# Kernel tuning notes

Measured on AMD Instinct MI355X. Metric: run time of the kernel, lower is better.

## Reference

```python
import jax, jax.numpy as jnp
import numpy as np

B, S, D_MODEL = 2, 1024, 512
HEAD = 8
DEPTH = D_MODEL // HEAD  # 64
NFEAT = 64


def _make_orf(rng, n_features, depth):
    # Mirrors OrthogonalRandomFeature: QR of uniform blocks, scaled by norms of gaussian rows.
    n, rem = divmod(n_features, depth)
    blocks = []
    for _ in range(n):
        q, _ = np.linalg.qr(rng.random((depth, depth)))
        blocks.append(q)
    if rem > 0:
        q, _ = np.linalg.qr(rng.random((depth, depth)))
        blocks.append(q[:rem])
    orf = np.concatenate(blocks, axis=0)
    mult = np.linalg.norm(rng.standard_normal((n_features, depth)), axis=1)
    return jnp.asarray(mult[:, None] * orf, dtype=jnp.float32)


def setup_inputs() -> dict:
    key = jax.random.key(0)
    ks = jax.random.split(key, 12)
    rng = np.random.default_rng(0)
    scale = 0.02
    inp = {
        "query": jax.random.normal(ks[0], (B, S, D_MODEL), dtype=jnp.float32),
        "key": jax.random.normal(ks[1], (B, S, D_MODEL), dtype=jnp.float32),
        "value": jax.random.normal(ks[2], (B, S, D_MODEL), dtype=jnp.float32),
        "Wq": jax.random.normal(ks[3], (DEPTH, DEPTH), dtype=jnp.float32) * scale,
        "bq": jnp.zeros((DEPTH,), dtype=jnp.float32),
        "Wk": jax.random.normal(ks[4], (DEPTH, DEPTH), dtype=jnp.float32) * scale,
        "bk": jnp.zeros((DEPTH,), dtype=jnp.float32),
        "Wv": jax.random.normal(ks[5], (DEPTH, DEPTH), dtype=jnp.float32) * scale,
        "bv": jnp.zeros((DEPTH,), dtype=jnp.float32),
        "orf_q": _make_orf(rng, NFEAT, DEPTH),
        "orf_k": _make_orf(rng, NFEAT, DEPTH),
        "Wfc": jax.random.normal(ks[6], (D_MODEL, D_MODEL), dtype=jnp.float32) * scale,
        "bfc": jnp.zeros((D_MODEL,), dtype=jnp.float32),
        "causal": 1,
    }
    return inp


def _kernel_fn(x, orf):
    # x: [n,h,s,d], orf: [f,d]; normalization uses ORF.shape[-1] = depth
    norm = 1.0 / (orf.shape[-1] ** 0.25)
    out = jnp.einsum('nhsd,fd->nhsf', x * norm, orf)
    return jax.nn.relu(out) + 0.001


def _causal_attention(q, k, v):
    # q,k: [n,h,s,f]; v: [n,h,s,d]
    k_cumsum = jnp.cumsum(k, axis=-2)                    # [n,h,s,f]
    x = jnp.einsum('nhkf,nhkd->nhkfd', k, v)             # [n,h,s,f,d]
    x = jnp.cumsum(x, axis=-3)
    x = x / k_cumsum[..., None]
    return jnp.einsum('nhqfd,nhqf->nhqd', x, q)          # [n,h,s,d]


def _bidirectional_attention(q, k, v):
    kt_i = jnp.sum(k, axis=-2)                           # [n,h,f]
    norm = 1.0 / jnp.einsum('nhqf,nhf->nhq', q, kt_i)    # [n,h,s]
    k_v = jnp.einsum('nhkf,nhkd->nhfd', k, v)            # [n,h,f,d]
    return jnp.einsum('nhfd,nhqf,nhq->nhqd', k_v, q, norm)


def reference(query, key, value, Wq, bq, Wk, bk, Wv, bv, orf_q, orf_k, Wfc, bfc, causal):
    b, s, _ = query.shape
    depth = Wq.shape[0]
    head = query.shape[-1] // depth
    # [b,s,d_model] -> [b,h,s,depth]
    q = query.reshape(b, s, head, depth).transpose(0, 2, 1, 3)
    k = key.reshape(b, s, head, depth).transpose(0, 2, 1, 3)
    v = value.reshape(b, s, head, depth).transpose(0, 2, 1, 3)
    # per-head Linear on depth (torch: x @ W.T + b)
    q = jnp.einsum('nhsd,ed->nhse', q, Wq) + bq
    k = jnp.einsum('nhsd,ed->nhse', k, Wk) + bk
    v = jnp.einsum('nhsd,ed->nhse', v, Wv) + bv
    q = _kernel_fn(q, orf_q)
    k = _kernel_fn(k, orf_k)
    if causal:
        out = _causal_attention(q, k, v)
    else:
        out = _bidirectional_attention(q, k, v)
    out = out.transpose(0, 2, 1, 3).reshape(b, s, head * depth)
    return jnp.einsum('nse,oe->nso', out, Wfc) + bfc
```

## Files before the change

### kernel.cpp

```cpp
#include <hip/hip_runtime.h>


#define BB 2
#define SS 1024
#define HH 8
#define DD 64
#define FF 64
#define DM 512
#define NCH 16

typedef __bf16 bf16_t;
typedef __attribute__((ext_vector_type(8))) __bf16 bf16x8;
typedef __attribute__((ext_vector_type(4))) __bf16 bf16x4;
typedef __attribute__((ext_vector_type(4))) float f32x4;

#define MFMA16(a,b,c) __builtin_amdgcn_mfma_f32_16x16x32_bf16((a),(b),(c),0,0,0)

__device__ inline bf16x8 cvt_f32x8(const float* p){
    const float4* p4 = (const float4*)p;
    float4 x = p4[0], y = p4[1];
    bf16x8 r;
    r[0]=(__bf16)x.x; r[1]=(__bf16)x.y; r[2]=(__bf16)x.z; r[3]=(__bf16)x.w;
    r[4]=(__bf16)y.x; r[5]=(__bf16)y.y; r[6]=(__bf16)y.z; r[7]=(__bf16)y.w;
    return r;
}

__global__ __launch_bounds__(256) void kfuse(
    const float* __restrict__ orf_q, const float* __restrict__ orf_k,
    const float* __restrict__ Wq, const float* __restrict__ bq,
    const float* __restrict__ Wk, const float* __restrict__ bk,
    const float* __restrict__ Wv, const float* __restrict__ Wfc,
    bf16_t* __restrict__ Mtq, bf16_t* __restrict__ Mtk,
    float* __restrict__ cq, float* __restrict__ ck,
    bf16_t* __restrict__ WvB, bf16_t* __restrict__ WfcB)
{
    const int tid = threadIdx.x, bid = blockIdx.x;
    if (bid < 2) {
        const float* ORF = bid ? orf_k : orf_q;
        const float* W   = bid ? Wk : Wq;
        const float* bb  = bid ? bk : bq;
        bf16_t* Mt = bid ? Mtk : Mtq;
        float* cc  = bid ? ck : cq;
        const float norm = 0.35355339059327373f;
        const int f = tid >> 2, d0 = (tid & 3) * 16;
        float acc[16];
        #pragma unroll
        for (int j=0;j<16;j++) acc[j]=0.f;
        float bacc = 0.f;
        for (int e=0;e<64;e++){
            float oe = ORF[f*64+e];
            const float* wr = W + e*64 + d0;
            #pragma unroll
            for (int j=0;j<16;j++) acc[j] += oe*wr[j];
            bacc += oe*bb[e];
        }
        #pragma unroll
        for (int j=0;j<16;j++) Mt[f*64+d0+j] = (__bf16)(norm*acc[j]);
        if ((tid&3)==0) cc[f] = norm*bacc;
    } else if (bid == 2) {
        for (int i=tid;i<4096;i+=256) WvB[i] = (__bf16)Wv[i];
    } else {
        const float4* W4 = (const float4*)Wfc;
        for (int i=(bid-3)*256+tid; i<65536; i+=13*256){
            float4 v = W4[i];
            bf16x4 o; o[0]=(__bf16)v.x; o[1]=(__bf16)v.y; o[2]=(__bf16)v.z; o[3]=(__bf16)v.w;
            *(bf16x4*)(WfcB + 4*i) = o;
        }
    }
}

__global__ __launch_bounds__(512) void kproj(
    const float* __restrict__ q_in, const float* __restrict__ k_in,
    const float* __restrict__ v_in,
    const bf16_t* __restrict__ Mtq, const float* __restrict__ cq,
    const bf16_t* __restrict__ Mtk, const float* __restrict__ ck,
    const bf16_t* __restrict__ WvB, const float* __restrict__ bv,
    bf16_t* __restrict__ PHI_Q, bf16_t* __restrict__ PHI_K,
    bf16_t* __restrict__ PHI_KT, bf16_t* __restrict__ VPT,
    float* __restrict__ CST, float* __restrict__ KCS)
{
    __shared__ bf16_t kt[64*72];
    __shared__ bf16_t vt[64*72];
    __shared__ float dsT[64*68];
    __shared__ float part[256];
    const int tid = threadIdx.x;
    const int l = tid & 63;
    const int w = __builtin_amdgcn_readfirstlane(tid >> 6);
    const int ww = w & 3;
    const int qd = l >> 4, m = l & 15;
    const int bid = blockIdx.x;
    const int bh = bid >> 4, ch = bid & 15;
    const int b = bh >> 3, h = bh & 7;
    const int s0 = ch*64;
    const int sw = s0 + ww*16;

    if (w < 4) {
        const float* xp = q_in + ((size_t)(b*SS + sw + m))*DM + h*DD;
        bf16x8 a0 = cvt_f32x8(xp + qd*8);
        bf16x8 a1 = cvt_f32x8(xp + 32 + qd*8);
        #pragma unroll
        for (int nt=0;nt<4;nt++){
            const int f = nt*16 + m;
            float cb = cq[f];
            f32x4 acc = {cb,cb,cb,cb};
            acc = MFMA16(a0, *(const bf16x8*)(Mtq + f*64 + qd*8), acc);
            acc = MFMA16(a1, *(const bf16x8*)(Mtq + f*64 + 32 + qd*8), acc);
            #pragma unroll
            for (int r=0;r<4;r++){
                float v = acc[r];
                v = (v>0.f)?v:0.f; v += 0.001f;
                PHI_Q[((size_t)bh*SS + sw + qd*4 + r)*FF + f] = (__bf16)v;
            }
        }
    } else {
        const float* xp = k_in + ((size_t)(b*SS + sw + m))*DM + h*DD;
        bf16x8 a0 = cvt_f32x8(xp + qd*8);
        bf16x8 a1 = cvt_f32x8(xp + 32 + qd*8);
        #pragma unroll
        for (int nt=0;nt<4;nt++){
            const int f = nt*16 + m;
            float cb = ck[f];
            f32x4 acc = {cb,cb,cb,cb};
            acc = MFMA16(a0, *(const bf16x8*)(Mtk + f*64 + qd*8), acc);
            acc = MFMA16(a1, *(const bf16x8*)(Mtk + f*64 + 32 + qd*8), acc);
            #pragma unroll
            for (int r=0;r<4;r++){
                float v = acc[r];
                v = (v>0.f)?v:0.f; v += 0.001f;
                __bf16 h16 = (__bf16)v;
                PHI_K[((size_t)bh*SS + sw + qd*4 + r)*FF + f] = h16;
                kt[f*72 + ww*16 + qd*4 + r] = h16;
            }
        }
    }
    __syncthreads();

    if (tid < 256) {
        const int f = tid >> 2, sg = tid & 3;
        bf16x8 v0 = *(bf16x8*)&kt[f*72 + sg*16];
        bf16x8 v1 = *(bf16x8*)&kt[f*72 + sg*16 + 8];
        bf16_t* dst = PHI_KT + ((size_t)bh*64 + f)*SS + s0 + sg*16;
        *(bf16x8*)dst = v0; *(bf16x8*)(dst+8) = v1;
    } else {
        const float* xp = v_in + ((size_t)(b*SS + sw + m))*DM + h*DD;
        bf16x8 a0 = cvt_f32x8(xp + qd*8);
        bf16x8 a1 = cvt_f32x8(xp + 32 + qd*8);
        #pragma unroll
        for (int nt=0;nt<4;nt++){
            const int e = nt*16 + m;
            float cb = bv[e];
            f32x4 acc = {cb,cb,cb,cb};
            acc = MFMA16(a0, *(const bf16x8*)(WvB + e*64 + qd*8), acc);
            acc = MFMA16(a1, *(const bf16x8*)(WvB + e*64 + 32 + qd*8), acc);
            #pragma unroll
            for (int r=0;r<4;r++)
                vt[e*72 + ww*16 + qd*4 + r] = (__bf16)acc[r];
        }
    }
    __syncthreads();

    {
        const int ft = ww, np = (w >> 2) * 2;
        bf16x8 a0 = *(bf16x8*)&kt[(ft*16+m)*72 + qd*8];
        bf16x8 a1 = *(bf16x8*)&kt[(ft*16+m)*72 + 32 + qd*8];
        #pragma unroll
        for (int j=0;j<2;j++){
            const int nt = np + j;
            f32x4 acc = {0.f,0.f,0.f,0.f};
            acc = MFMA16(a0, *(bf16x8*)&vt[(nt*16+m)*72 + qd*8], acc);
            acc = MFMA16(a1, *(bf16x8*)&vt[(nt*16+m)*72 + 32 + qd*8], acc);
            #pragma unroll
            for (int r=0;r<4;r++)
                dsT[(nt*16+m)*68 + ft*16 + qd*4 + r] = acc[r];
        }
    }
    if (tid < 256) {
        const int d = tid >> 2, sg = tid & 3;
        bf16x8 v0 = *(bf16x8*)&vt[d*72 + sg*16];
        bf16x8 v1 = *(bf16x8*)&vt[d*72 + sg*16 + 8];
        bf16_t* dst = VPT + ((size_t)bh*64 + d)*SS + s0 + sg*16;
        *(bf16x8*)dst = v0; *(bf16x8*)(dst+8) = v1;
    } else {
        const int t2 = tid - 256;
        const int f = t2 & 63, sg = t2 >> 6;
        bf16x8 x0 = *(bf16x8*)&kt[f*72 + sg*16];
        bf16x8 x1 = *(bf16x8*)&kt[f*72 + sg*16 + 8];
        float sm = 0.f;
        #pragma unroll
        for (int j=0;j<8;j++) sm += (float)x0[j] + (float)x1[j];
        part[sg*64 + f] = sm;
    }
    __syncthreads();

    if (tid < 256) {
        const int d = tid >> 2, F = (tid & 3) * 16;
        float* dst = CST + ((size_t)bid*64 + d)*64 + F;
        #pragma unroll
        for (int j=0;j<4;j++)
            *(float4*)(dst + 4*j) = *(float4*)&dsT[d*68 + F + 4*j];
    } else if (tid < 320) {
        const int f = tid - 256;
        KCS[(size_t)bid*64 + f] = part[f] + part[64+f] + part[128+f] + part[192+f];
    }
}

__global__ __launch_bounds__(256) void kprefix(float* __restrict__ CST, float* __restrict__ KCS)
{
    const int tid = threadIdx.x, bid = blockIdx.x;
    const int bh = bid >> 2, q = bid & 3;
    const int e4 = q*256 + tid;
    float4 vals[16];
    #pragma unroll
    for (int c = 0; c < NCH; c++)
        vals[c] = ((float4*)(CST + ((size_t)(bh*NCH + c))*4096))[e4];
    float4 run = make_float4(0.f, 0.f, 0.f, 0.f);
    #pragma unroll
    for (int c = 0; c < NCH; c++) {
        ((float4*)(CST + ((size_t)(bh*NCH + c))*4096))[e4] = run;
        run.x += vals[c].x; run.y += vals[c].y; run.z += vals[c].z; run.w += vals[c].w;
    }
    if (q == 0 && tid < 64) {
        float kv[16];
        #pragma unroll
        for (int c = 0; c < NCH; c++) kv[c] = KCS[((size_t)(bh*NCH + c))*64 + tid];
        float r = 0.f;
        #pragma unroll
        for (int c = 0; c < NCH; c++) { KCS[((size_t)(bh*NCH + c))*64 + tid] = r; r += kv[c]; }
    }
}

__global__ __launch_bounds__(512) void kattn(
    const bf16_t* __restrict__ PHI_Q, const bf16_t* __restrict__ PHI_K,
    const bf16_t* __restrict__ PHI_KT, const bf16_t* __restrict__ VPT,
    const float* __restrict__ CST, const float* __restrict__ KCS,
    bf16_t* __restrict__ O)
{
    __shared__ float kct[64*67];
    __shared__ bf16_t qnl[64*72];
    __shared__ bf16_t sAl[64*72];
    __shared__ float scanp[256];
    const int tid = threadIdx.x;
    const int l = tid & 63;
    const int w = __builtin_amdgcn_readfirstlane(tid >> 6);
    const int rt = w & 3;
    const int np = (w >> 2) * 2;
    const int qd = l >> 4, m = l & 15;
    const int bid = blockIdx.x;
    const int bh = bid >> 4, ch = bid & 15;
    const int cs0 = ch*64;

    if (tid < 256) {
        const int f = tid >> 2, sg = tid & 3;
        const bf16_t* kp = PHI_KT + ((size_t)bh*64 + f)*SS + cs0 + sg*16;
        bf16x8 x0 = *(const bf16x8*)kp;
        bf16x8 x1 = *(const bf16x8*)(kp+8);
        #pragma unroll
        for (int j=0;j<8;j++){
            kct[f*67 + sg*16 + j]     = (float)x0[j];
            kct[f*67 + sg*16 + 8 + j] = (float)x1[j];
        }
    }
    __syncthreads();

    const int f2 = tid >> 2, sg2 = tid & 3;
    float v16[16];
    if (tid < 256) {
        #pragma unroll
        for (int j=0;j<16;j++) v16[j] = kct[f2*67 + sg2*16 + j];
        #pragma unroll
        for (int j=1;j<16;j++) v16[j] += v16[j-1];
        scanp[f2*4 + sg2] = v16[15];
    }
    __syncthreads();
    if (tid < 256) {
        float offs = KCS[(size_t)bid*64 + f2];
        if (sg2 > 0) offs += scanp[f2*4 + 0];
        if (sg2 > 1) offs += scanp[f2*4 + 1];
        if (sg2 > 2) offs += scanp[f2*4 + 2];
        #pragma unroll
        for (int j=0;j<16;j++) kct[f2*67 + sg2*16 + j] = offs + v16[j];
    }
    __syncthreads();

    if (tid < 256) {
        const int sr = tid >> 2, F = (tid & 3) * 16;
        const bf16_t* qp = PHI_Q + ((size_t)bh*SS + cs0 + sr)*FF + F;
        bf16x8 x0 = *(const bf16x8*)qp;
        bf16x8 x1 = *(const bf16x8*)(qp+8);
        bf16x8 o0, o1;
        #pragma unroll
        for (int j=0;j<8;j++){
            o0[j] = (__bf16)((float)x0[j] / kct[(F+j)*67 + sr]);
            o1[j] = (__bf16)((float)x1[j] / kct[(F+8+j)*67 + sr]);
        }
        *(bf16x8*)&qnl[sr*72 + F]     = o0;
        *(bf16x8*)&qnl[sr*72 + F + 8] = o1;
    }
    __syncthreads();

    bf16x8 qa0 = *(bf16x8*)&qnl[(rt*16+m)*72 + qd*8];
    bf16x8 qa1 = *(bf16x8*)&qnl[(rt*16+m)*72 + 32 + qd*8];

    #pragma unroll
    for (int j=0;j<2;j++){
        const int nt = np + j;
        const bf16_t* kb = PHI_K + ((size_t)bh*SS + cs0 + nt*16 + m)*FF;
        f32x4 acc = {0.f,0.f,0.f,0.f};
        acc = MFMA16(qa0, *(const bf16x8*)(kb + qd*8), acc);
        acc = MFMA16(qa1, *(const bf16x8*)(kb + 32 + qd*8), acc);
        const int t_loc = nt*16 + m;
        #pragma unroll
        for (int r=0;r<4;r++){
            const int s_loc = rt*16 + qd*4 + r;
            float v = (t_loc <= s_loc) ? acc[r] : 0.f;
            sAl[s_loc*72 + t_loc] = (__bf16)v;
        }
    }
    __syncthreads();

    bf16x8 sa0 = *(bf16x8*)&sAl[(rt*16+m)*72 + qd*8];
    bf16x8 sa1 = *(bf16x8*)&sAl[(rt*16+m)*72 + 32 + qd*8];

    #pragma unroll
    for (int j=0;j<2;j++){
        const int nt = np + j;
        const int d = nt*16 + m;
        const bf16_t* vb = VPT + ((size_t)bh*64 + d)*SS + cs0;
        const float* pp = CST + ((size_t)bid*64 + d)*64;
        f32x4 acc = {0.f,0.f,0.f,0.f};
        acc = MFMA16(sa0, *(const bf16x8*)(vb + qd*8), acc);
        acc = MFMA16(sa1, *(const bf16x8*)(vb + 32 + qd*8), acc);
        acc = MFMA16(qa0, cvt_f32x8(pp + qd*8), acc);
        acc = MFMA16(qa1, cvt_f32x8(pp + 32 + qd*8), acc);
        #pragma unroll
        for (int r=0;r<4;r++)
            O[((size_t)bh*SS + cs0 + rt*16 + qd*4 + r)*DD + d] = (__bf16)acc[r];
    }
}

__global__ __launch_bounds__(512) void kfc(
    const bf16_t* __restrict__ O, const bf16_t* __restrict__ WfcB,
    const float* __restrict__ bfc, float* __restrict__ out)
{
    const int tid = threadIdx.x;
    const int l = tid & 63;
    const int w = __builtin_amdgcn_readfirstlane(tid >> 6);
    const int rw = w & 3, cpair = (w >> 2) * 2;
    const int qd = l >> 4, m = l & 15;
    const int bid = blockIdx.x;
    const int rb = bid >> 3, cb = bid & 7;
    const int r0 = rb*64 + rw*16;

    f32x4 acc[2];
    #pragma unroll
    for (int j=0;j<2;j++){
        float bb = bfc[cb*64 + (cpair+j)*16 + m];
        acc[j][0]=bb; acc[j][1]=bb; acc[j][2]=bb; acc[j][3]=bb;
    }
    const int row = r0 + m;
    const int b = row >> 10, s = row & 1023;
    #pragma unroll 4
    for (int c=0;c<16;c++){
        const int h = c >> 1;
        const int doff = (c & 1)*32 + qd*8;
        bf16x8 a = *(const bf16x8*)(O + ((size_t)((b*HH + h)*SS + s))*DD + doff);
        #pragma unroll
        for (int j=0;j<2;j++){
            bf16x8 bfr = *(const bf16x8*)(WfcB + (size_t)(cb*64 + (cpair+j)*16 + m)*DM + c*32 + qd*8);
            acc[j] = MFMA16(a, bfr, acc[j]);
        }
    }
    #pragma unroll
    for (int j=0;j<2;j++){
        #pragma unroll
        for (int r=0;r<4;r++){
            const int rr = r0 + qd*4 + r;
            out[(size_t)rr*DM + cb*64 + (cpair+j)*16 + m] = acc[j][r];
        }
    }
}

extern "C" void kernel_launch(void* const* d_in, const int* in_sizes, int n_in,
                              void* d_out, int out_size, void* d_ws, size_t ws_size,
                              hipStream_t stream) {
    const float* q_in  = (const float*)d_in[0];
    const float* k_in  = (const float*)d_in[1];
    const float* v_in  = (const float*)d_in[2];
    const float* Wq    = (const float*)d_in[3];
    const float* bq    = (const float*)d_in[4];
    const float* Wk    = (const float*)d_in[5];
    const float* bk    = (const float*)d_in[6];
    const float* Wv    = (const float*)d_in[7];
    const float* bv    = (const float*)d_in[8];
    const float* orf_q = (const float*)d_in[9];
    const float* orf_k = (const float*)d_in[10];
    const float* Wfc   = (const float*)d_in[11];
    const float* bfc   = (const float*)d_in[12];

    float* CST   = (float*)d_ws;
    float* KCS   = CST + 1048576;
    float* cq    = KCS + 16384;
    float* ck    = cq + 64;
    bf16_t* PHI_Q  = (bf16_t*)(ck + 64);
    bf16_t* PHI_K  = PHI_Q + 1048576;
    bf16_t* PHI_KT = PHI_K + 1048576;
    bf16_t* VPT    = PHI_KT + 1048576;
    bf16_t* O      = VPT + 1048576;
    bf16_t* Mtq    = O + 1048576;
    bf16_t* Mtk    = Mtq + 4096;
    bf16_t* WvB    = Mtk + 4096;
    bf16_t* WfcB   = WvB + 4096;

    kfuse<<<16, 256, 0, stream>>>(orf_q, orf_k, Wq, bq, Wk, bk, Wv, Wfc,
                                  Mtq, Mtk, cq, ck, WvB, WfcB);
    kproj<<<256, 512, 0, stream>>>(q_in, k_in, v_in, Mtq, cq, Mtk, ck, WvB, bv,
                                   PHI_Q, PHI_K, PHI_KT, VPT, CST, KCS);
    kprefix<<<64, 256, 0, stream>>>(CST, KCS);
    kattn<<<256, 512, 0, stream>>>(PHI_Q, PHI_K, PHI_KT, VPT, CST, KCS, O);
    kfc<<<256, 512, 0, stream>>>(O, WfcB, bfc, (float*)d_out);
}
```

Baseline: 134.0 us.

## Fuse all five kernels into one persistent kernel with grid-wide atomic barriers

```diff
diff --git a/kernel.cpp b/kernel.cpp
--- a/kernel.cpp
+++ b/kernel.cpp
@@ -1,7 +1,6 @@
 #include <hip/hip_runtime.h>
 
 
-#define BB 2
 #define SS 1024
 #define HH 8
 #define DD 64
@@ -16,73 +15,55 @@
 
 #define MFMA16(a,b,c) __builtin_amdgcn_mfma_f32_16x16x32_bf16((a),(b),(c),0,0,0)
 
-__device__ inline bf16x8 cvt_f32x8(const float* p){
-    const float4* p4 = (const float4*)p;
-    float4 x = p4[0], y = p4[1];
+__device__ inline bf16x8 pack8(float4 x, float4 y){
     bf16x8 r;
     r[0]=(__bf16)x.x; r[1]=(__bf16)x.y; r[2]=(__bf16)x.z; r[3]=(__bf16)x.w;
     r[4]=(__bf16)y.x; r[5]=(__bf16)y.y; r[6]=(__bf16)y.z; r[7]=(__bf16)y.w;
     return r;
 }
-
-__global__ __launch_bounds__(256) void kfuse(
-    const float* __restrict__ orf_q, const float* __restrict__ orf_k,
+__device__ inline bf16x8 cvt_f32x8(const float* p){
+    const float4* p4 = (const float4*)p;
+    return pack8(p4[0], p4[1]);
+}
+
+__device__ inline void gsync(unsigned* cnt, int slot){
+    __syncthreads();
+    if (threadIdx.x == 0){
+        __threadfence();
+        __hip_atomic_fetch_add(cnt + slot, 1u, __ATOMIC_ACQ_REL, __HIP_MEMORY_SCOPE_AGENT);
+        while (__hip_atomic_load(cnt + slot, __ATOMIC_ACQUIRE, __HIP_MEMORY_SCOPE_AGENT) < 256u)
+            __builtin_amdgcn_s_sleep(2);
+        __threadfence();
+    }
+    __syncthreads();
+}
+
+__global__ __launch_bounds__(512, 2) void kfused(
+    const float* __restrict__ q_in, const float* __restrict__ k_in,
+    const float* __restrict__ v_in,
     const float* __restrict__ Wq, const float* __restrict__ bq,
     const float* __restrict__ Wk, const float* __restrict__ bk,
-    const float* __restrict__ Wv, const float* __restrict__ Wfc,
+    const float* __restrict__ Wv, const float* __restrict__ bv,
+    const float* __restrict__ orf_q, const float* __restrict__ orf_k,
+    const float* __restrict__ Wfc, const float* __restrict__ bfc,
     bf16_t* __restrict__ Mtq, bf16_t* __restrict__ Mtk,
     float* __restrict__ cq, float* __restrict__ ck,
-    bf16_t* __restrict__ WvB, bf16_t* __restrict__ WfcB)
+    bf16_t* __restrict__ WvB, bf16_t* __restrict__ WfcB,
+    float* __restrict__ CST, float* __restrict__ KCS,
+    bf16_t* __restrict__ O, unsigned* __restrict__ syncc,
+    float* __restrict__ out)
 {
-    const int tid = threadIdx.x, bid = blockIdx.x;
-    if (bid < 2) {
-        const float* ORF = bid ? orf_k : orf_q;
-        const float* W   = bid ? Wk : Wq;
-        const float* bb  = bid ? bk : bq;
-        bf16_t* Mt = bid ? Mtk : Mtq;
-        float* cc  = bid ? ck : cq;
-        const float norm = 0.35355339059327373f;
-        const int f = tid >> 2, d0 = (tid & 3) * 16;
-        float acc[16];
-        #pragma unroll
-        for (int j=0;j<16;j++) acc[j]=0.f;
-        float bacc = 0.f;
-        for (int e=0;e<64;e++){
-            float oe = ORF[f*64+e];
-            const float* wr = W + e*64 + d0;
-            #pragma unroll
-            for (int j=0;j<16;j++) acc[j] += oe*wr[j];
-            bacc += oe*bb[e];
-        }
-        #pragma unroll
-        for (int j=0;j<16;j++) Mt[f*64+d0+j] = (__bf16)(norm*acc[j]);
-        if ((tid&3)==0) cc[f] = norm*bacc;
-    } else if (bid == 2) {
-        for (int i=tid;i<4096;i+=256) WvB[i] = (__bf16)Wv[i];
-    } else {
-        const float4* W4 = (const float4*)Wfc;
-        for (int i=(bid-3)*256+tid; i<65536; i+=13*256){
-            float4 v = W4[i];
-            bf16x4 o; o[0]=(__bf16)v.x; o[1]=(__bf16)v.y; o[2]=(__bf16)v.z; o[3]=(__bf16)v.w;
-            *(bf16x4*)(WfcB + 4*i) = o;
-        }
-    }
-}
-
-__global__ __launch_bounds__(512) void kproj(
-    const float* __restrict__ q_in, const float* __restrict__ k_in,
-    const float* __restrict__ v_in,
-    const bf16_t* __restrict__ Mtq, const float* __restrict__ cq,
-    const bf16_t* __restrict__ Mtk, const float* __restrict__ ck,
-    const bf16_t* __restrict__ WvB, const float* __restrict__ bv,
-    bf16_t* __restrict__ PHI_Q, bf16_t* __restrict__ PHI_K,
-    bf16_t* __restrict__ PHI_KT, bf16_t* __restrict__ VPT,
-    float* __restrict__ CST, float* __restrict__ KCS)
-{
-    __shared__ bf16_t kt[64*72];
-    __shared__ bf16_t vt[64*72];
-    __shared__ float dsT[64*68];
-    __shared__ float part[256];
+    __shared__ __align__(16) char smem[64512];
+    float*  dsT  = (float*)smem;
+    float*  kct  = (float*)smem;
+    bf16_t* kt   = (bf16_t*)(smem + 17408);
+    bf16_t* sAl  = (bf16_t*)(smem + 17408);
+    bf16_t* vt   = (bf16_t*)(smem + 26624);
+    bf16_t* qnl  = (bf16_t*)(smem + 35840);
+    bf16_t* phql = (bf16_t*)(smem + 45056);
+    bf16_t* phkl = (bf16_t*)(smem + 54272);
+    float*  part = (float*)(smem + 63488);
+
     const int tid = threadIdx.x;
     const int l = tid & 63;
     const int w = __builtin_amdgcn_readfirstlane(tid >> 6);
@@ -94,71 +75,110 @@
     const int s0 = ch*64;
     const int sw = s0 + ww*16;
 
-    if (w < 4) {
-        const float* xp = q_in + ((size_t)(b*SS + sw + m))*DM + h*DD;
-        bf16x8 a0 = cvt_f32x8(xp + qd*8);
-        bf16x8 a1 = cvt_f32x8(xp + 32 + qd*8);
-        #pragma unroll
-        for (int nt=0;nt<4;nt++){
-            const int f = nt*16 + m;
-            float cb = cq[f];
-            f32x4 acc = {cb,cb,cb,cb};
-            acc = MFMA16(a0, *(const bf16x8*)(Mtq + f*64 + qd*8), acc);
-            acc = MFMA16(a1, *(const bf16x8*)(Mtq + f*64 + 32 + qd*8), acc);
-            #pragma unroll
-            for (int r=0;r<4;r++){
-                float v = acc[r];
-                v = (v>0.f)?v:0.f; v += 0.001f;
-                PHI_Q[((size_t)bh*SS + sw + qd*4 + r)*FF + f] = (__bf16)v;
-            }
-        }
-    } else {
-        const float* xp = k_in + ((size_t)(b*SS + sw + m))*DM + h*DD;
-        bf16x8 a0 = cvt_f32x8(xp + qd*8);
-        bf16x8 a1 = cvt_f32x8(xp + 32 + qd*8);
-        #pragma unroll
-        for (int nt=0;nt<4;nt++){
-            const int f = nt*16 + m;
-            float cb = ck[f];
-            f32x4 acc = {cb,cb,cb,cb};
-            acc = MFMA16(a0, *(const bf16x8*)(Mtk + f*64 + qd*8), acc);
-            acc = MFMA16(a1, *(const bf16x8*)(Mtk + f*64 + 32 + qd*8), acc);
-            #pragma unroll
-            for (int r=0;r<4;r++){
-                float v = acc[r];
-                v = (v>0.f)?v:0.f; v += 0.001f;
-                __bf16 h16 = (__bf16)v;
-                PHI_K[((size_t)bh*SS + sw + qd*4 + r)*FF + f] = h16;
-                kt[f*72 + ww*16 + qd*4 + r] = h16;
-            }
-        }
-    }
-    __syncthreads();
-
-    if (tid < 256) {
-        const int f = tid >> 2, sg = tid & 3;
-        bf16x8 v0 = *(bf16x8*)&kt[f*72 + sg*16];
-        bf16x8 v1 = *(bf16x8*)&kt[f*72 + sg*16 + 8];
-        bf16_t* dst = PHI_KT + ((size_t)bh*64 + f)*SS + s0 + sg*16;
-        *(bf16x8*)dst = v0; *(bf16x8*)(dst+8) = v1;
-    } else {
-        const float* xp = v_in + ((size_t)(b*SS + sw + m))*DM + h*DD;
-        bf16x8 a0 = cvt_f32x8(xp + qd*8);
-        bf16x8 a1 = cvt_f32x8(xp + 32 + qd*8);
+    const float* xrow = ((w < 4) ? q_in : k_in) + ((size_t)(b*SS + sw + m))*DM + h*DD;
+    float4 pA0 = *(const float4*)(xrow + qd*8);
+    float4 pA1 = *(const float4*)(xrow + qd*8 + 4);
+    float4 pB0 = *(const float4*)(xrow + 32 + qd*8);
+    float4 pB1 = *(const float4*)(xrow + 32 + qd*8 + 4);
+    float4 vA0 = {0,0,0,0}, vA1 = {0,0,0,0}, vB0 = {0,0,0,0}, vB1 = {0,0,0,0};
+    if (w >= 4){
+        const float* vrow = v_in + ((size_t)(b*SS + sw + m))*DM + h*DD;
+        vA0 = *(const float4*)(vrow + qd*8);
+        vA1 = *(const float4*)(vrow + qd*8 + 4);
+        vB0 = *(const float4*)(vrow + 32 + qd*8);
+        vB1 = *(const float4*)(vrow + 32 + qd*8 + 4);
+    }
+
+    if (bid < 2){
+        if (tid < 256){
+            const float* ORF = bid ? orf_k : orf_q;
+            const float* W   = bid ? Wk : Wq;
+            const float* bb  = bid ? bk : bq;
+            bf16_t* Mt = bid ? Mtk : Mtq;
+            float* cc  = bid ? ck : cq;
+            const float norm = 0.35355339059327373f;
+            const int f = tid >> 2, d0 = (tid & 3) * 16;
+            float acc[16];
+            #pragma unroll
+            for (int j=0;j<16;j++) acc[j]=0.f;
+            float bacc = 0.f;
+            for (int e=0;e<64;e++){
+                float oe = ORF[f*64+e];
+                const float* wr = W + e*64 + d0;
+                #pragma unroll
+                for (int j=0;j<16;j++) acc[j] += oe*wr[j];
+                bacc += oe*bb[e];
+            }
+            #pragma unroll
+            for (int j=0;j<16;j++) Mt[f*64+d0+j] = (__bf16)(norm*acc[j]);
+            if ((tid&3)==0) cc[f] = norm*bacc;
+        }
+    } else if (bid == 2){
+        for (int i=tid;i<4096;i+=512) WvB[i] = (__bf16)Wv[i];
+    } else if (bid < 16){
+        const float4* W4 = (const float4*)Wfc;
+        for (int i=(bid-3)*512+tid; i<65536; i+=13*512){
+            float4 v = W4[i];
+            bf16x4 o; o[0]=(__bf16)v.x; o[1]=(__bf16)v.y; o[2]=(__bf16)v.z; o[3]=(__bf16)v.w;
+            *(bf16x4*)(WfcB + 4*i) = o;
+        }
+    }
+    gsync(syncc, 0);
+
+    {
+        bf16x8 a0 = pack8(pA0, pA1);
+        bf16x8 a1 = pack8(pB0, pB1);
+        if (w < 4){
+            #pragma unroll
+            for (int nt=0;nt<4;nt++){
+                const int f = nt*16 + m;
+                float cb = cq[f];
+                f32x4 acc = {cb,cb,cb,cb};
+                acc = MFMA16(a0, *(const bf16x8*)(Mtq + f*64 + qd*8), acc);
+                acc = MFMA16(a1, *(const bf16x8*)(Mtq + f*64 + 32 + qd*8), acc);
+                #pragma unroll
+                for (int r=0;r<4;r++){
+                    float v = acc[r];
+                    v = (v>0.f)?v:0.f; v += 0.001f;
+                    phql[(ww*16 + qd*4 + r)*72 + f] = (__bf16)v;
+                }
+            }
+        } else {
+            #pragma unroll
+            for (int nt=0;nt<4;nt++){
+                const int f = nt*16 + m;
+                float cb = ck[f];
+                f32x4 acc = {cb,cb,cb,cb};
+                acc = MFMA16(a0, *(const bf16x8*)(Mtk + f*64 + qd*8), acc);
+                acc = MFMA16(a1, *(const bf16x8*)(Mtk + f*64 + 32 + qd*8), acc);
+                #pragma unroll
+                for (int r=0;r<4;r++){
+                    float v = acc[r];
+                    v = (v>0.f)?v:0.f; v += 0.001f;
+                    __bf16 h16 = (__bf16)v;
+                    kt[f*72 + ww*16 + qd*4 + r] = h16;
+                    phkl[(ww*16 + qd*4 + r)*72 + f] = h16;
+                }
+            }
+        }
+    }
+    __syncthreads();
+    if (w >= 4){
+        bf16x8 va0 = pack8(vA0, vA1);
+        bf16x8 va1 = pack8(vB0, vB1);
         #pragma unroll
         for (int nt=0;nt<4;nt++){
             const int e = nt*16 + m;
             float cb = bv[e];
             f32x4 acc = {cb,cb,cb,cb};
-            acc = MFMA16(a0, *(const bf16x8*)(WvB + e*64 + qd*8), acc);
-            acc = MFMA16(a1, *(const bf16x8*)(WvB + e*64 + 32 + qd*8), acc);
+            acc = MFMA16(va0, *(const bf16x8*)(WvB + e*64 + qd*8), acc);
+            acc = MFMA16(va1, *(const bf16x8*)(WvB + e*64 + 32 + qd*8), acc);
             #pragma unroll
             for (int r=0;r<4;r++)
                 vt[e*72 + ww*16 + qd*4 + r] = (__bf16)acc[r];
         }
     }
     __syncthreads();
-
     {
         const int ft = ww, np = (w >> 2) * 2;
         bf16x8 a0 = *(bf16x8*)&kt[(ft*16+m)*72 + qd*8];
@@ -174,13 +194,7 @@
                 dsT[(nt*16+m)*68 + ft*16 + qd*4 + r] = acc[r];
         }
     }
-    if (tid < 256) {
-        const int d = tid >> 2, sg = tid & 3;
-        bf16x8 v0 = *(bf16x8*)&vt[d*72 + sg*16];
-        bf16x8 v1 = *(bf16x8*)&vt[d*72 + sg*16 + 8];
-        bf16_t* dst = VPT + ((size_t)bh*64 + d)*SS + s0 + sg*16;
-        *(bf16x8*)dst = v0; *(bf16x8*)(dst+8) = v1;
-    } else {
+    if (tid >= 256){
         const int t2 = tid - 256;
         const int f = t2 & 63, sg = t2 >> 6;
         bf16x8 x0 = *(bf16x8*)&kt[f*72 + sg*16];
@@ -191,69 +205,45 @@
         part[sg*64 + f] = sm;
     }
     __syncthreads();
-
-    if (tid < 256) {
+    if (tid < 256){
         const int d = tid >> 2, F = (tid & 3) * 16;
         float* dst = CST + ((size_t)bid*64 + d)*64 + F;
         #pragma unroll
         for (int j=0;j<4;j++)
             *(float4*)(dst + 4*j) = *(float4*)&dsT[d*68 + F + 4*j];
-    } else if (tid < 320) {
+    } else if (tid < 320){
         const int f = tid - 256;
         KCS[(size_t)bid*64 + f] = part[f] + part[64+f] + part[128+f] + part[192+f];
     }
-}
-
-__global__ __launch_bounds__(256) void kprefix(float* __restrict__ CST, float* __restrict__ KCS)
-{
-    const int tid = threadIdx.x, bid = blockIdx.x;
-    const int bh = bid >> 2, q = bid & 3;
-    const int e4 = q*256 + tid;
-    float4 vals[16];
-    #pragma unroll
-    for (int c = 0; c < NCH; c++)
-        vals[c] = ((float4*)(CST + ((size_t)(bh*NCH + c))*4096))[e4];
-    float4 run = make_float4(0.f, 0.f, 0.f, 0.f);
-    #pragma unroll
-    for (int c = 0; c < NCH; c++) {
-        ((float4*)(CST + ((size_t)(bh*NCH + c))*4096))[e4] = run;
-        run.x += vals[c].x; run.y += vals[c].y; run.z += vals[c].z; run.w += vals[c].w;
-    }
-    if (q == 0 && tid < 64) {
+    gsync(syncc, 1);
+
+    if (tid < 64){
+        const int e4 = ch*64 + tid;
+        float4 vals[16];
+        #pragma unroll
+        for (int c=0;c<NCH;c++)
+            vals[c] = ((float4*)(CST + ((size_t)(bh*NCH + c))*4096))[e4];
+        float4 run = {0.f,0.f,0.f,0.f};
+        #pragma unroll
+        for (int c=0;c<NCH;c++){
+            ((float4*)(CST + ((size_t)(bh*NCH + c))*4096))[e4] = run;
+            run.x += vals[c].x; run.y += vals[c].y; run.z += vals[c].z; run.w += vals[c].w;
+        }
+    } else if (ch == 0 && tid < 128){
+        const int f = tid - 64;
         float kv[16];
         #pragma unroll
-        for (int c = 0; c < NCH; c++) kv[c] = KCS[((size_t)(bh*NCH + c))*64 + tid];
+        for (int c=0;c<NCH;c++) kv[c] = KCS[((size_t)(bh*NCH + c))*64 + f];
         float r = 0.f;
         #pragma unroll
-        for (int c = 0; c < NCH; c++) { KCS[((size_t)(bh*NCH + c))*64 + tid] = r; r += kv[c]; }
-    }
-}
-
-__global__ __launch_bounds__(512) void kattn(
-    const bf16_t* __restrict__ PHI_Q, const bf16_t* __restrict__ PHI_K,
-    const bf16_t* __restrict__ PHI_KT, const bf16_t* __restrict__ VPT,
-    const float* __restrict__ CST, const float* __restrict__ KCS,
-    bf16_t* __restrict__ O)
-{
-    __shared__ float kct[64*67];
-    __shared__ bf16_t qnl[64*72];
-    __shared__ bf16_t sAl[64*72];
-    __shared__ float scanp[256];
-    const int tid = threadIdx.x;
-    const int l = tid & 63;
-    const int w = __builtin_amdgcn_readfirstlane(tid >> 6);
-    const int rt = w & 3;
-    const int np = (w >> 2) * 2;
-    const int qd = l >> 4, m = l & 15;
-    const int bid = blockIdx.x;
-    const int bh = bid >> 4, ch = bid & 15;
-    const int cs0 = ch*64;
-
-    if (tid < 256) {
+        for (int c=0;c<NCH;c++){ KCS[((size_t)(bh*NCH + c))*64 + f] = r; r += kv[c]; }
+    }
+    gsync(syncc, 2);
+
+    if (tid < 256){
         const int f = tid >> 2, sg = tid & 3;
-        const bf16_t* kp = PHI_KT + ((size_t)bh*64 + f)*SS + cs0 + sg*16;
-        bf16x8 x0 = *(const bf16x8*)kp;
-        bf16x8 x1 = *(const bf16x8*)(kp+8);
+        bf16x8 x0 = *(bf16x8*)&kt[f*72 + sg*16];
+        bf16x8 x1 = *(bf16x8*)&kt[f*72 + sg*16 + 8];
         #pragma unroll
         for (int j=0;j<8;j++){
             kct[f*67 + sg*16 + j]     = (float)x0[j];
@@ -261,32 +251,31 @@
         }
     }
     __syncthreads();
-
-    const int f2 = tid >> 2, sg2 = tid & 3;
-    float v16[16];
-    if (tid < 256) {
-        #pragma unroll
-        for (int j=0;j<16;j++) v16[j] = kct[f2*67 + sg2*16 + j];
-        #pragma unroll
-        for (int j=1;j<16;j++) v16[j] += v16[j-1];
-        scanp[f2*4 + sg2] = v16[15];
-    }
-    __syncthreads();
-    if (tid < 256) {
-        float offs = KCS[(size_t)bid*64 + f2];
-        if (sg2 > 0) offs += scanp[f2*4 + 0];
-        if (sg2 > 1) offs += scanp[f2*4 + 1];
-        if (sg2 > 2) offs += scanp[f2*4 + 2];
-        #pragma unroll
-        for (int j=0;j<16;j++) kct[f2*67 + sg2*16 + j] = offs + v16[j];
-    }
-    __syncthreads();
-
-    if (tid < 256) {
+    {
+        const int f2 = tid >> 2, sg2 = tid & 3;
+        float v16[16];
+        if (tid < 256){
+            #pragma unroll
+            for (int j=0;j<16;j++) v16[j] = kct[f2*67 + sg2*16 + j];
+            #pragma unroll
+            for (int j=1;j<16;j++) v16[j] += v16[j-1];
+            part[f2*4 + sg2] = v16[15];
+        }
+        __syncthreads();
+        if (tid < 256){
+            float offs = KCS[(size_t)bid*64 + f2];
+            if (sg2 > 0) offs += part[f2*4 + 0];
+            if (sg2 > 1) offs += part[f2*4 + 1];
+            if (sg2 > 2) offs += part[f2*4 + 2];
+            #pragma unroll
+            for (int j=0;j<16;j++) kct[f2*67 + sg2*16 + j] = offs + v16[j];
+        }
+    }
+    __syncthreads();
+    if (tid < 256){
         const int sr = tid >> 2, F = (tid & 3) * 16;
-        const bf16_t* qp = PHI_Q + ((size_t)bh*SS + cs0 + sr)*FF + F;
-        bf16x8 x0 = *(const bf16x8*)qp;
-        bf16x8 x1 = *(const bf16x8*)(qp+8);
+        bf16x8 x0 = *(bf16x8*)&phql[sr*72 + F];
+        bf16x8 x1 = *(bf16x8*)&phql[sr*72 + F + 8];
         bf16x8 o0, o1;
         #pragma unroll
         for (int j=0;j<8;j++){
@@ -298,16 +287,16 @@
     }
     __syncthreads();
 
+    const int rt = ww, np = (w >> 2) * 2;
     bf16x8 qa0 = *(bf16x8*)&qnl[(rt*16+m)*72 + qd*8];
     bf16x8 qa1 = *(bf16x8*)&qnl[(rt*16+m)*72 + 32 + qd*8];
 
     #pragma unroll
     for (int j=0;j<2;j++){
         const int nt = np + j;
-        const bf16_t* kb = PHI_K + ((size_t)bh*SS + cs0 + nt*16 + m)*FF;
         f32x4 acc = {0.f,0.f,0.f,0.f};
-        acc = MFMA16(qa0, *(const bf16x8*)(kb + qd*8), acc);
-        acc = MFMA16(qa1, *(const bf16x8*)(kb + 32 + qd*8), acc);
+        acc = MFMA16(qa0, *(const bf16x8*)&phkl[(nt*16+m)*72 + qd*8], acc);
+        acc = MFMA16(qa1, *(const bf16x8*)&phkl[(nt*16+m)*72 + 32 + qd*8], acc);
         const int t_loc = nt*16 + m;
         #pragma unroll
         for (int r=0;r<4;r++){
@@ -318,64 +307,56 @@
     }
     __syncthreads();
 
-    bf16x8 sa0 = *(bf16x8*)&sAl[(rt*16+m)*72 + qd*8];
-    bf16x8 sa1 = *(bf16x8*)&sAl[(rt*16+m)*72 + 32 + qd*8];
-
-    #pragma unroll
-    for (int j=0;j<2;j++){
-        const int nt = np + j;
-        const int d = nt*16 + m;
-        const bf16_t* vb = VPT + ((size_t)bh*64 + d)*SS + cs0;
-        const float* pp = CST + ((size_t)bid*64 + d)*64;
-        f32x4 acc = {0.f,0.f,0.f,0.f};
-        acc = MFMA16(sa0, *(const bf16x8*)(vb + qd*8), acc);
-        acc = MFMA16(sa1, *(const bf16x8*)(vb + 32 + qd*8), acc);
-        acc = MFMA16(qa0, cvt_f32x8(pp + qd*8), acc);
-        acc = MFMA16(qa1, cvt_f32x8(pp + 32 + qd*8), acc);
-        #pragma unroll
-        for (int r=0;r<4;r++)
-            O[((size_t)bh*SS + cs0 + rt*16 + qd*4 + r)*DD + d] = (__bf16)acc[r];
-    }
-}
-
-__global__ __launch_bounds__(512) void kfc(
-    const bf16_t* __restrict__ O, const bf16_t* __restrict__ WfcB,
-    const float* __restrict__ bfc, float* __restrict__ out)
-{
-    const int tid = threadIdx.x;
-    const int l = tid & 63;
-    const int w = __builtin_amdgcn_readfirstlane(tid >> 6);
-    const int rw = w & 3, cpair = (w >> 2) * 2;
-    const int qd = l >> 4, m = l & 15;
-    const int bid = blockIdx.x;
-    const int rb = bid >> 3, cb = bid & 7;
-    const int r0 = rb*64 + rw*16;
-
-    f32x4 acc[2];
-    #pragma unroll
-    for (int j=0;j<2;j++){
-        float bb = bfc[cb*64 + (cpair+j)*16 + m];
-        acc[j][0]=bb; acc[j][1]=bb; acc[j][2]=bb; acc[j][3]=bb;
-    }
-    const int row = r0 + m;
-    const int b = row >> 10, s = row & 1023;
-    #pragma unroll 4
-    for (int c=0;c<16;c++){
-        const int h = c >> 1;
-        const int doff = (c & 1)*32 + qd*8;
-        bf16x8 a = *(const bf16x8*)(O + ((size_t)((b*HH + h)*SS + s))*DD + doff);
+    {
+        bf16x8 sa0 = *(bf16x8*)&sAl[(rt*16+m)*72 + qd*8];
+        bf16x8 sa1 = *(bf16x8*)&sAl[(rt*16+m)*72 + 32 + qd*8];
         #pragma unroll
         for (int j=0;j<2;j++){
-            bf16x8 bfr = *(const bf16x8*)(WfcB + (size_t)(cb*64 + (cpair+j)*16 + m)*DM + c*32 + qd*8);
-            acc[j] = MFMA16(a, bfr, acc[j]);
-        }
-    }
-    #pragma unroll
-    for (int j=0;j<2;j++){
-        #pragma unroll
-        for (int r=0;r<4;r++){
-            const int rr = r0 + qd*4 + r;
-            out[(size_t)rr*DM + cb*64 + (cpair+j)*16 + m] = acc[j][r];
+            const int nt = np + j;
+            const int d = nt*16 + m;
+            const float* pp = CST + ((size_t)bid*64 + d)*64;
+            f32x4 acc = {0.f,0.f,0.f,0.f};
+            acc = MFMA16(sa0, *(const bf16x8*)&vt[d*72 + qd*8], acc);
+            acc = MFMA16(sa1, *(const bf16x8*)&vt[d*72 + 32 + qd*8], acc);
+            acc = MFMA16(qa0, cvt_f32x8(pp + qd*8), acc);
+            acc = MFMA16(qa1, cvt_f32x8(pp + 32 + qd*8), acc);
+            #pragma unroll
+            for (int r=0;r<4;r++)
+                O[((size_t)bh*SS + s0 + rt*16 + qd*4 + r)*DD + d] = (__bf16)acc[r];
+        }
+    }
+    gsync(syncc, 3);
+
+    {
+        const int rb = bid >> 3, cb = bid & 7;
+        const int rw = ww, cpair = (w >> 2) * 2;
+        const int r0 = rb*64 + rw*16;
+        f32x4 acc[2];
+        #pragma unroll
+        for (int j=0;j<2;j++){
+            float bb = bfc[cb*64 + (cpair+j)*16 + m];
+            acc[j][0]=bb; acc[j][1]=bb; acc[j][2]=bb; acc[j][3]=bb;
+        }
+        const int row = r0 + m;
+        const int b2 = row >> 10, s2 = row & 1023;
+        #pragma unroll 4
+        for (int c=0;c<16;c++){
+            const int hc = c >> 1;
+            const int doff = (c & 1)*32 + qd*8;
+            bf16x8 a = *(const bf16x8*)(O + ((size_t)((b2*HH + hc)*SS + s2))*DD + doff);
+            #pragma unroll
+            for (int j=0;j<2;j++){
+                bf16x8 bfr = *(const bf16x8*)(WfcB + (size_t)(cb*64 + (cpair+j)*16 + m)*DM + c*32 + qd*8);
+                acc[j] = MFMA16(a, bfr, acc[j]);
+            }
+        }
+        #pragma unroll
+        for (int j=0;j<2;j++){
+            #pragma unroll
+            for (int r=0;r<4;r++){
+                const int rr = r0 + qd*4 + r;
+                out[(size_t)rr*DM + cb*64 + (cpair+j)*16 + m] = acc[j][r];
+            }
         }
     }
 }
@@ -397,25 +378,20 @@
     const float* Wfc   = (const float*)d_in[11];
     const float* bfc   = (const float*)d_in[12];
 
-    float* CST   = (float*)d_ws;
-    float* KCS   = CST + 1048576;
-    float* cq    = KCS + 16384;
-    float* ck    = cq + 64;
-    bf16_t* PHI_Q  = (bf16_t*)(ck + 64);
-    bf16_t* PHI_K  = PHI_Q + 1048576;
-    bf16_t* PHI_KT = PHI_K + 1048576;
-    bf16_t* VPT    = PHI_KT + 1048576;
-    bf16_t* O      = VPT + 1048576;
-    bf16_t* Mtq    = O + 1048576;
-    bf16_t* Mtk    = Mtq + 4096;
-    bf16_t* WvB    = Mtk + 4096;
-    bf16_t* WfcB   = WvB + 4096;
-
-    kfuse<<<16, 256, 0, stream>>>(orf_q, orf_k, Wq, bq, Wk, bk, Wv, Wfc,
-                                  Mtq, Mtk, cq, ck, WvB, WfcB);
-    kproj<<<256, 512, 0, stream>>>(q_in, k_in, v_in, Mtq, cq, Mtk, ck, WvB, bv,
-                                   PHI_Q, PHI_K, PHI_KT, VPT, CST, KCS);
-    kprefix<<<64, 256, 0, stream>>>(CST, KCS);
-    kattn<<<256, 512, 0, stream>>>(PHI_Q, PHI_K, PHI_KT, VPT, CST, KCS, O);
-    kfc<<<256, 512, 0, stream>>>(O, WfcB, bfc, (float*)d_out);
-}
+    unsigned* syncc = (unsigned*)d_ws;
+    float* CST  = (float*)d_ws + 64;
+    float* KCS  = CST + 1048576;
+    float* cq   = KCS + 16384;
+    float* ck   = cq + 64;
+    bf16_t* Mtq  = (bf16_t*)(ck + 64);
+    bf16_t* Mtk  = Mtq + 4096;
+    bf16_t* WvB  = Mtk + 4096;
+    bf16_t* WfcB = WvB + 4096;
+    bf16_t* O    = WfcB + 262144;
+
+    hipMemsetAsync(d_ws, 0, 256, stream);
+    hipLaunchKernelGGL(kfused, dim3(256), dim3(512), 0, stream,
+                       q_in, k_in, v_in, Wq, bq, Wk, bk, Wv, bv, orf_q, orf_k,
+                       Wfc, bfc, Mtq, Mtk, cq, ck, WvB, WfcB, CST, KCS, O,
+                       syncc, (float*)d_out);
+}
```

After: 246.8 us. 84.1% more time.

## Fuse chunk prefix-sum into attention kernel, dropping separate kprefix launch

Applied to the files above, without the earlier changes.

```diff
diff --git a/kernel.cpp b/kernel.cpp
--- a/kernel.cpp
+++ b/kernel.cpp
@@ -1,7 +1,6 @@
 #include <hip/hip_runtime.h>
 
 
-#define BB 2
 #define SS 1024
 #define HH 8
 #define DD 64
@@ -204,31 +203,6 @@
     }
 }
 
-__global__ __launch_bounds__(256) void kprefix(float* __restrict__ CST, float* __restrict__ KCS)
-{
-    const int tid = threadIdx.x, bid = blockIdx.x;
-    const int bh = bid >> 2, q = bid & 3;
-    const int e4 = q*256 + tid;
-    float4 vals[16];
-    #pragma unroll
-    for (int c = 0; c < NCH; c++)
-        vals[c] = ((float4*)(CST + ((size_t)(bh*NCH + c))*4096))[e4];
-    float4 run = make_float4(0.f, 0.f, 0.f, 0.f);
-    #pragma unroll
-    for (int c = 0; c < NCH; c++) {
-        ((float4*)(CST + ((size_t)(bh*NCH + c))*4096))[e4] = run;
-        run.x += vals[c].x; run.y += vals[c].y; run.z += vals[c].z; run.w += vals[c].w;
-    }
-    if (q == 0 && tid < 64) {
-        float kv[16];
-        #pragma unroll
-        for (int c = 0; c < NCH; c++) kv[c] = KCS[((size_t)(bh*NCH + c))*64 + tid];
-        float r = 0.f;
-        #pragma unroll
-        for (int c = 0; c < NCH; c++) { KCS[((size_t)(bh*NCH + c))*64 + tid] = r; r += kv[c]; }
-    }
-}
-
 __global__ __launch_bounds__(512) void kattn(
     const bf16_t* __restrict__ PHI_Q, const bf16_t* __restrict__ PHI_K,
     const bf16_t* __restrict__ PHI_KT, const bf16_t* __restrict__ VPT,
@@ -238,7 +212,9 @@
     __shared__ float kct[64*67];
     __shared__ bf16_t qnl[64*72];
     __shared__ bf16_t sAl[64*72];
+    __shared__ bf16_t pT[64*72];
     __shared__ float scanp[256];
+    __shared__ float kcsp[64];
     const int tid = threadIdx.x;
     const int l = tid & 63;
     const int w = __builtin_amdgcn_readfirstlane(tid >> 6);
@@ -249,7 +225,27 @@
     const int bh = bid >> 4, ch = bid & 15;
     const int cs0 = ch*64;
 
-    if (tid < 256) {
+    if (tid >= 256) {
+        const int t2 = tid - 256;
+        const int base = t2 * 16;
+        const int d = t2 >> 2, f0 = (t2 & 3) * 16;
+        float acc[16];
+        #pragma unroll
+        for (int j=0;j<16;j++) acc[j]=0.f;
+        for (int cc = 0; cc < ch; cc++) {
+            const float4* p = (const float4*)(CST + ((size_t)(bh*NCH + cc))*4096 + base);
+            #pragma unroll
+            for (int j=0;j<4;j++){
+                float4 t = p[j];
+                acc[4*j]+=t.x; acc[4*j+1]+=t.y; acc[4*j+2]+=t.z; acc[4*j+3]+=t.w;
+            }
+        }
+        bf16x8 o0, o1;
+        #pragma unroll
+        for (int j=0;j<8;j++){ o0[j]=(__bf16)acc[j]; o1[j]=(__bf16)acc[8+j]; }
+        *(bf16x8*)&pT[d*72 + f0]     = o0;
+        *(bf16x8*)&pT[d*72 + f0 + 8] = o1;
+    } else {
         const int f = tid >> 2, sg = tid & 3;
         const bf16_t* kp = PHI_KT + ((size_t)bh*64 + f)*SS + cs0 + sg*16;
         bf16x8 x0 = *(const bf16x8*)kp;
@@ -259,6 +255,11 @@
             kct[f*67 + sg*16 + j]     = (float)x0[j];
             kct[f*67 + sg*16 + 8 + j] = (float)x1[j];
         }
+        if (tid < 64) {
+            float r = 0.f;
+            for (int cc = 0; cc < ch; cc++) r += KCS[((size_t)(bh*NCH + cc))*64 + tid];
+            kcsp[tid] = r;
+        }
     }
     __syncthreads();
 
@@ -273,7 +274,7 @@
     }
     __syncthreads();
     if (tid < 256) {
-        float offs = KCS[(size_t)bid*64 + f2];
+        float offs = kcsp[f2];
         if (sg2 > 0) offs += scanp[f2*4 + 0];
         if (sg2 > 1) offs += scanp[f2*4 + 1];
         if (sg2 > 2) offs += scanp[f2*4 + 2];
@@ -326,12 +327,11 @@
         const int nt = np + j;
         const int d = nt*16 + m;
         const bf16_t* vb = VPT + ((size_t)bh*64 + d)*SS + cs0;
-        const float* pp = CST + ((size_t)bid*64 + d)*64;
         f32x4 acc = {0.f,0.f,0.f,0.f};
         acc = MFMA16(sa0, *(const bf16x8*)(vb + qd*8), acc);
         acc = MFMA16(sa1, *(const bf16x8*)(vb + 32 + qd*8), acc);
-        acc = MFMA16(qa0, cvt_f32x8(pp + qd*8), acc);
-        acc = MFMA16(qa1, cvt_f32x8(pp + 32 + qd*8), acc);
+        acc = MFMA16(qa0, *(const bf16x8*)&pT[d*72 + qd*8], acc);
+        acc = MFMA16(qa1, *(const bf16x8*)&pT[d*72 + 32 + qd*8], acc);
         #pragma unroll
         for (int r=0;r<4;r++)
             O[((size_t)bh*SS + cs0 + rt*16 + qd*4 + r)*DD + d] = (__bf16)acc[r];
@@ -415,7 +415,6 @@
                                   Mtq, Mtk, cq, ck, WvB, WfcB);
     kproj<<<256, 512, 0, stream>>>(q_in, k_in, v_in, Mtq, cq, Mtk, ck, WvB, bv,
                                    PHI_Q, PHI_K, PHI_KT, VPT, CST, KCS);
-    kprefix<<<64, 256, 0, stream>>>(CST, KCS);
     kattn<<<256, 512, 0, stream>>>(PHI_Q, PHI_K, PHI_KT, VPT, CST, KCS, O);
     kfc<<<256, 512, 0, stream>>>(O, WfcB, bfc, (float*)d_out);
 }
```

Measured after the change: 133.2 us. About the same (-0.6%).
